# Performance work log

Hardware: AMD Instinct MI355X
Metric: run time of the kernel (lower is better)

Reference implementation:

```python
import jax, jax.numpy as jnp
import numpy as np
from jax import lax

B, C, H, W = 8, 128, 128, 128
HEADS = 16
HEAD_C = C // HEADS  # 8
SLOPE = 0.2
EPS = 1e-12


def _conv(x, w, b, padding, groups=1):
    # x: [B,C,H,W], w: [O,I/groups,kh,kw]
    y = lax.conv_general_dilated(
        x, w, window_strides=(1, 1), padding=padding,
        dimension_numbers=("NCHW", "OIHW", "NCHW"),
        feature_group_count=groups)
    return y + b[None, :, None, None]


def _conv_block(x, conv1_w, conv1_b, conv2_w, conv2_b, dw_w, dw_b, sc_w, sc_b):
    h = _conv(x, conv1_w, conv1_b, ((1, 1), (1, 1)))            # 3x3, zero pad
    h = jnp.where(h >= 0, h, SLOPE * h)                          # LeakyReLU
    h = _conv(h, conv2_w, conv2_b, ((0, 0), (0, 0)))             # 1x1
    hp = jnp.pad(h, ((0, 0), (0, 0), (1, 1), (1, 1)), mode="reflect")
    h = _conv(hp, dw_w, dw_b, ((0, 0), (0, 0)), groups=C)        # depthwise 3x3, reflect pad
    h = jnp.where(h >= 0, h, SLOPE * h)
    sc = _conv(x, sc_w, sc_b, ((0, 0), (0, 0)))                  # 1x1 shortcut
    return h + sc


def setup_inputs() -> dict:
    key = jax.random.key(0)
    ks = jax.random.split(key, 10)
    s = 0.05
    return {
        "x1": jax.random.normal(ks[0], (B, C, H, W), jnp.float32),
        "x2": jax.random.normal(ks[1], (B, C, H, W), jnp.float32),
        "temperature": jnp.ones((HEADS, 1, 1), jnp.float32),
        "conv1_w": jax.random.normal(ks[2], (C, C, 3, 3), jnp.float32) * s,
        "conv1_b": jnp.zeros((C,), jnp.float32),
        "conv2_w": jax.random.normal(ks[3], (C, C, 1, 1), jnp.float32) * s,
        "conv2_b": jnp.zeros((C,), jnp.float32),
        "dw_w": jax.random.normal(ks[4], (C, 1, 3, 3), jnp.float32) * s,
        "dw_b": jnp.zeros((C,), jnp.float32),
        "sc_w": jax.random.normal(ks[5], (C, C, 1, 1), jnp.float32) * s,
        "sc_b": jnp.zeros((C,), jnp.float32),
    }


def reference(x1, x2, temperature, conv1_w, conv1_b, conv2_w, conv2_b,
              dw_w, dw_b, sc_w, sc_b):
    b, c, h, w = x2.shape
    # b (head c) h w -> b head c (h w)
    qk = x1.reshape(b, HEADS, HEAD_C, h * w)
    v = x2.reshape(b, HEADS, HEAD_C, h * w)
    # L2-normalize over spatial dim (F.normalize, eps=1e-12)
    norm = jnp.sqrt(jnp.sum(qk * qk, axis=-1, keepdims=True))
    qn = qk / jnp.maximum(norm, EPS)
    # channel attention: [b, head, c, c]
    attn = jnp.einsum("bhcn,bhdn->bhcd", qn, qn) * temperature
    attn = jax.nn.softmax(attn, axis=-1)
    out = jnp.einsum("bhcd,bhdn->bhcn", attn, v)
    out = out.reshape(b, c, h, w)
    out = _conv_block(out, conv1_w, conv1_b, conv2_w, conv2_b,
                      dw_w, dw_b, sc_w, sc_b)
    return out + x1
```

## Files before the change

### kernel.cpp

```cpp
#include <hip/hip_runtime.h>
#include <hip/hip_bf16.h>

typedef __attribute__((ext_vector_type(8))) short short8;
typedef __attribute__((ext_vector_type(4))) float f32x4;

#define NB 8
#define NC 128
#define NHW 128
#define NSP (NHW*NHW)
#define SLOPE 0.2f
#define EPSN 1e-12f

static __device__ __forceinline__ unsigned short f2bf(float f) {
    __hip_bfloat16 h = __float2bfloat16(f);
    return *reinterpret_cast<unsigned short*>(&h);
}
static __device__ __forceinline__ float bf2f(__hip_bfloat16 h) {
    return __bfloat162float(h);
}

__global__ void prep_wb1(const float* __restrict__ w, __hip_bfloat16* __restrict__ wb) {
    int idx = blockIdx.x * 256 + threadIdx.x;
    if (idx >= 128 * 128 * 9) return;
    int kw = idx % 3; int t = idx / 3;
    int kh = t % 3;   t /= 3;
    int i  = t % 128; int o = t / 128;
    int tap = kh * 3 + kw;
    int q = i >> 5, lk = (i >> 3) & 3, j = i & 7;
    int wn = o >> 6, c = (o >> 4) & 3, l15 = o & 15;
    int lane = lk * 16 + l15;
    size_t chunk = ((size_t)(tap * 4 + q) * 2 + wn) * 4 + c;
    wb[chunk * 512 + lane * 8 + j] = __float2bfloat16(w[idx]);
}

__global__ void prep_w1x1(const float* __restrict__ w, __hip_bfloat16* __restrict__ wb) {
    int idx = blockIdx.x * 256 + threadIdx.x;
    if (idx >= 128 * 128) return;
    int i = idx & 127, o = idx >> 7;
    int kk = i >> 5, lk = (i >> 3) & 3, j = i & 7;
    int wn = o >> 6, c = (o >> 4) & 3, l15 = o & 15;
    int lane = lk * 16 + l15;
    size_t chunk = ((size_t)(wn * 4 + kk) * 4 + c);
    wb[chunk * 512 + lane * 8 + j] = __float2bfloat16(w[idx]);
}

__global__ __launch_bounds__(256) void gram_part(const float* __restrict__ x1,
                                                 float* __restrict__ Gp) {
    int bh = blockIdx.x & 127;
    int q  = blockIdx.x >> 7;
    const float* base = x1 + (size_t)bh * 8 * NSP + q * 4096;
    float acc[8][8];
#pragma unroll
    for (int c = 0; c < 8; c++)
#pragma unroll
        for (int d = 0; d < 8; d++) acc[c][d] = 0.f;

    for (int n = threadIdx.x; n < 4096; n += 256) {
        float v[8];
#pragma unroll
        for (int c = 0; c < 8; c++) v[c] = base[c * NSP + n];
#pragma unroll
        for (int c = 0; c < 8; c++)
#pragma unroll
            for (int d = 0; d < 8; d++)
                acc[c][d] = fmaf(v[c], v[d], acc[c][d]);
    }
#pragma unroll
    for (int c = 0; c < 8; c++)
#pragma unroll
        for (int d = 0; d < 8; d++)
            for (int off = 32; off > 0; off >>= 1)
                acc[c][d] += __shfl_down(acc[c][d], off);

    __shared__ float red[4][64];
    int wv = threadIdx.x >> 6;
    if ((threadIdx.x & 63) == 0) {
#pragma unroll
        for (int c = 0; c < 8; c++)
#pragma unroll
            for (int d = 0; d < 8; d++) red[wv][c * 8 + d] = acc[c][d];
    }
    __syncthreads();
    if (threadIdx.x < 64)
        Gp[(size_t)(q * 128 + bh) * 64 + threadIdx.x] =
            red[0][threadIdx.x] + red[1][threadIdx.x] + red[2][threadIdx.x] + red[3][threadIdx.x];
}

__global__ void gram_reduce(const float* __restrict__ Gp, float* __restrict__ G) {
    int bh = blockIdx.x;
    int t = threadIdx.x;
    float s = 0.f;
#pragma unroll
    for (int q = 0; q < 4; q++) s += Gp[(size_t)(q * 128 + bh) * 64 + t];
    G[bh * 64 + t] = s;
}

__global__ void softmax_kernel(const float* __restrict__ G, const float* __restrict__ temp,
                               float* __restrict__ attn) {
    int bh = blockIdx.x; int h = bh & 15;
    int t = threadIdx.x;
    int c = t >> 3, d = t & 7;
    const float* g = G + bh * 64;
    float nc = fmaxf(sqrtf(g[c * 8 + c]), EPSN);
    float nd = fmaxf(sqrtf(g[d * 8 + d]), EPSN);
    float a = g[t] / (nc * nd) * temp[h];
    float m = a;
#pragma unroll
    for (int off = 4; off > 0; off >>= 1) m = fmaxf(m, __shfl_xor(m, off));
    float e = __expf(a - m);
    float s = e;
#pragma unroll
    for (int off = 4; off > 0; off >>= 1) s += __shfl_xor(s, off);
    attn[bh * 64 + t] = e / s;
}

__global__ __launch_bounds__(256) void av_v2(const float* __restrict__ x2,
                                             const float* __restrict__ attn,
                                             __hip_bfloat16* __restrict__ yt) {
    int b  = blockIdx.x >> 8;
    int p0 = (blockIdx.x & 255) << 6;
    __shared__ float vt[128][65];
    __shared__ float at[16][65];
    for (int idx = threadIdx.x; idx < 1024; idx += 256)
        at[idx >> 6][idx & 63] = attn[(size_t)b * 1024 + idx];
    for (int idx = threadIdx.x; idx < 8192; idx += 256) {
        int row = idx >> 6, col = idx & 63;
        vt[row][col] = x2[(size_t)(b * 128 + row) * NSP + p0 + col];
    }
    __syncthreads();
    for (int idx = threadIdx.x; idx < 1024; idx += 256) {
        int cq = idx & 15;
        int p  = idx >> 4;
        float vv[8];
#pragma unroll
        for (int d = 0; d < 8; d++) vv[d] = vt[cq * 8 + d][p];
        unsigned int pk[4];
#pragma unroll
        for (int c = 0; c < 8; c += 2) {
            float s0 = 0.f, s1 = 0.f;
#pragma unroll
            for (int d = 0; d < 8; d++) {
                s0 = fmaf(at[cq][c * 8 + d], vv[d], s0);
                s1 = fmaf(at[cq][(c + 1) * 8 + d], vv[d], s1);
            }
            pk[c >> 1] = (unsigned int)f2bf(s0) | ((unsigned int)f2bf(s1) << 16);
        }
        uint4 st; st.x = pk[0]; st.y = pk[1]; st.z = pk[2]; st.w = pk[3];
        *reinterpret_cast<uint4*>(yt + ((size_t)b * NSP + p0 + p) * 128 + cq * 8) = st;
    }
}

__global__ __launch_bounds__(256, 4) void fused_conv(const __hip_bfloat16* __restrict__ yt,
                                                     const __hip_bfloat16* __restrict__ wb1,
                                                     const __hip_bfloat16* __restrict__ wb2,
                                                     const __hip_bfloat16* __restrict__ wbsc,
                                                     const float* __restrict__ b1,
                                                     const float* __restrict__ b2,
                                                     const float* __restrict__ bsc,
                                                     const float* __restrict__ x1,
                                                     __hip_bfloat16* __restrict__ h2,
                                                     float* __restrict__ out) {
    __shared__ uint4 smem[2048];
    char* smem_raw = (char*)smem;
    int bid = blockIdx.x;
    int blk = (bid & 7) * 128 + (bid >> 3);
    int b = blk >> 7, h = blk & 127;
    int tid = threadIdx.x;
    int lane = tid & 63;
    int wid = tid >> 6;
    int wm = wid >> 1, wn = wid & 1;
    int l15 = lane & 15;
    int lk = lane >> 4;

    const short8* wf1  = reinterpret_cast<const short8*>(wb1);
    const short8* wf2  = reinterpret_cast<const short8*>(wb2);
    const short8* wfsc = reinterpret_cast<const short8*>(wbsc);

    f32x4 acc[4][4];
#pragma unroll
    for (int a = 0; a < 4; a++)
#pragma unroll
        for (int c = 0; c < 4; c++) acc[a][c] = (f32x4){0.f, 0.f, 0.f, 0.f};

#pragma unroll
    for (int q = 0; q < 4; ++q) {
        __syncthreads();
        for (int idx = tid; idx < 1584; idx += 256) {
            int g = idx & 3;
            int colr = idx >> 2;
            int col = colr % 132;
            int r = colr / 132;
            int hh = h + r - 1;
            int w = col - 1;
            uint4 v = make_uint4(0u, 0u, 0u, 0u);
            if ((unsigned)hh < 128u && (unsigned)w < 128u)
                v = *reinterpret_cast<const uint4*>(
                    yt + (((size_t)(b * 128 + hh)) * 128 + w) * 128 + q * 32 + g * 8);
            smem[r * 528 + col * 4 + (g ^ (col & 3))] = v;
        }
        __syncthreads();

#pragma unroll
        for (int tap = 0; tap < 9; ++tap) {
            int kh = tap / 3, kw = tap - kh * 3;
            const short8* wp = wf1 + ((size_t)((tap * 4 + q) * 2 + wn) * 4) * 64 + lane;
            short8 bfr[4];
#pragma unroll
            for (int c = 0; c < 4; ++c)
                bfr[c] = wp[c * 64];
            short8 afr[4];
#pragma unroll
            for (int a = 0; a < 4; ++a) {
                int col = (wm * 4 + a) * 16 + l15 + kw;
                afr[a] = *reinterpret_cast<const short8*>(
                    &smem[kh * 528 + col * 4 + (lk ^ (col & 3))]);
            }
#pragma unroll
            for (int a = 0; a < 4; ++a)
#pragma unroll
                for (int c = 0; c < 4; ++c)
                    acc[a][c] = __builtin_amdgcn_mfma_f32_16x16x32_bf16(
                        afr[a], bfr[c], acc[a][c], 0, 0, 0);
        }
    }

    __syncthreads();
#pragma unroll
    for (int c = 0; c < 4; ++c) {
        int o = wn * 64 + c * 16 + l15;
        float bv = b1[o];
        int go = o >> 3, ob = (o & 7) << 1;
#pragma unroll
        for (int a = 0; a < 4; ++a) {
            int pb = (wm * 4 + a) * 16 + lk * 4;
#pragma unroll
            for (int j = 0; j < 4; ++j) {
                int p = pb + j;
                float v = acc[a][c][j] + bv;
                v = v >= 0.f ? v : SLOPE * v;
                *reinterpret_cast<__hip_bfloat16*>(
                    smem_raw + p * 256 + (((go ^ (p & 15)) << 4) | ob)) = __float2bfloat16(v);
            }
        }
    }
    __syncthreads();

#pragma unroll
    for (int a = 0; a < 4; a++)
#pragma unroll
        for (int c = 0; c < 4; c++) acc[a][c] = (f32x4){0.f, 0.f, 0.f, 0.f};
#pragma unroll
    for (int kk = 0; kk < 4; ++kk) {
        short8 bfr[4];
#pragma unroll
        for (int c = 0; c < 4; ++c)
            bfr[c] = wf2[((size_t)(wn * 4 + kk) * 4 + c) * 64 + lane];
        short8 afr[4];
        int g = kk * 4 + lk;
#pragma unroll
        for (int a = 0; a < 4; ++a) {
            int p = (wm * 4 + a) * 16 + l15;
            afr[a] = *reinterpret_cast<const short8*>(smem_raw + p * 256 + ((g ^ (p & 15)) << 4));
        }
#pragma unroll
        for (int a = 0; a < 4; ++a)
#pragma unroll
            for (int c = 0; c < 4; ++c)
                acc[a][c] = __builtin_amdgcn_mfma_f32_16x16x32_bf16(afr[a], bfr[c], acc[a][c], 0, 0, 0);
    }
#pragma unroll
    for (int c = 0; c < 4; ++c) {
        int o = wn * 64 + c * 16 + l15;
        float bv = b2[o];
        size_t obase = ((size_t)(b * 128 + o) * 128 + h) * 128;
#pragma unroll
        for (int a = 0; a < 4; ++a) {
            int w0 = (wm * 4 + a) * 16 + lk * 4;
            uint2 st;
            st.x = (unsigned int)f2bf(acc[a][c][0] + bv) | ((unsigned int)f2bf(acc[a][c][1] + bv) << 16);
            st.y = (unsigned int)f2bf(acc[a][c][2] + bv) | ((unsigned int)f2bf(acc[a][c][3] + bv) << 16);
            *reinterpret_cast<uint2*>(h2 + obase + w0) = st;
        }
    }

    __syncthreads();
    for (int idx = tid; idx < 2048; idx += 256) {
        int p = idx >> 4, g = idx & 15;
        uint4 v = *reinterpret_cast<const uint4*>(
            yt + ((size_t)(b * NSP + h * 128 + p)) * 128 + g * 8);
        *reinterpret_cast<uint4*>(smem_raw + p * 256 + ((g ^ (p & 15)) << 4)) = v;
    }
    __syncthreads();

#pragma unroll
    for (int a = 0; a < 4; a++)
#pragma unroll
        for (int c = 0; c < 4; c++) acc[a][c] = (f32x4){0.f, 0.f, 0.f, 0.f};
#pragma unroll
    for (int kk = 0; kk < 4; ++kk) {
        short8 bfr[4];
#pragma unroll
        for (int c = 0; c < 4; ++c)
            bfr[c] = wfsc[((size_t)(wn * 4 + kk) * 4 + c) * 64 + lane];
        short8 afr[4];
        int g = kk * 4 + lk;
#pragma unroll
        for (int a = 0; a < 4; ++a) {
            int p = (wm * 4 + a) * 16 + l15;
            afr[a] = *reinterpret_cast<const short8*>(smem_raw + p * 256 + ((g ^ (p & 15)) << 4));
        }
#pragma unroll
        for (int a = 0; a < 4; ++a)
#pragma unroll
            for (int c = 0; c < 4; ++c)
                acc[a][c] = __builtin_amdgcn_mfma_f32_16x16x32_bf16(afr[a], bfr[c], acc[a][c], 0, 0, 0);
    }
#pragma unroll
    for (int c = 0; c < 4; ++c) {
        int o = wn * 64 + c * 16 + l15;
        float bv = bsc[o];
        size_t obase = ((size_t)(b * 128 + o) * 128 + h) * 128;
#pragma unroll
        for (int a = 0; a < 4; ++a) {
            int w0 = (wm * 4 + a) * 16 + lk * 4;
            float4 xv = *reinterpret_cast<const float4*>(x1 + obase + w0);
            float4 st;
            st.x = acc[a][c][0] + bv + xv.x;
            st.y = acc[a][c][1] + bv + xv.y;
            st.z = acc[a][c][2] + bv + xv.z;
            st.w = acc[a][c][3] + bv + xv.w;
            *reinterpret_cast<float4*>(out + obase + w0) = st;
        }
    }
}

__global__ __launch_bounds__(256) void dw_v2(const __hip_bfloat16* __restrict__ h2,
                                             const float* __restrict__ dww,
                                             const float* __restrict__ dwb,
                                             float* __restrict__ out) {
    int bid = blockIdx.x;
    int swz = (bid & 7) * 1024 + (bid >> 3);
    size_t tidx = (size_t)swz * 256 + threadIdx.x;
    int w0 = (int)((tidx & 15) << 3);
    int hh = (int)((tidx >> 4) & 127);
    int bc = (int)(tidx >> 11);
    int c  = bc & 127;
    const __hip_bfloat16* src = h2 + ((size_t)bc << 14);
    float wg[9];
#pragma unroll
    for (int k = 0; k < 9; ++k) wg[k] = dww[c * 9 + k];
    float bv = dwb[c];
    float a8[8];
#pragma unroll
    for (int j = 0; j < 8; ++j) a8[j] = bv;
#pragma unroll
    for (int kh = 0; kh < 3; ++kh) {
        int ih = hh + kh - 1;
        ih = ih < 0 ? 1 : (ih > 127 ? 126 : ih);
        const __hip_bfloat16* row = src + ih * 128;
        short8 mid = *reinterpret_cast<const short8*>(row + w0);
        float v[10];
        v[0] = bf2f(row[w0 == 0 ? 1 : w0 - 1]);
#pragma unroll
        for (int j = 0; j < 8; ++j)
            v[j + 1] = __uint_as_float((unsigned int)(unsigned short)mid[j] << 16);
        v[9] = bf2f(row[w0 == 120 ? 126 : w0 + 8]);
#pragma unroll
        for (int kw = 0; kw < 3; ++kw)
#pragma unroll
            for (int j = 0; j < 8; ++j)
                a8[j] = fmaf(v[j + kw], wg[kh * 3 + kw], a8[j]);
    }
    size_t ob = ((size_t)bc << 14) + hh * 128 + w0;
    float4 o0 = *reinterpret_cast<const float4*>(out + ob);
    float4 o1 = *reinterpret_cast<const float4*>(out + ob + 4);
#pragma unroll
    for (int j = 0; j < 8; ++j) a8[j] = a8[j] >= 0.f ? a8[j] : SLOPE * a8[j];
    o0.x += a8[0]; o0.y += a8[1]; o0.z += a8[2]; o0.w += a8[3];
    o1.x += a8[4]; o1.y += a8[5]; o1.z += a8[6]; o1.w += a8[7];
    *reinterpret_cast<float4*>(out + ob) = o0;
    *reinterpret_cast<float4*>(out + ob + 4) = o1;
}

extern "C" void kernel_launch(void* const* d_in, const int* in_sizes, int n_in,
                              void* d_out, int out_size, void* d_ws, size_t ws_size,
                              hipStream_t stream) {
    const float* x1   = (const float*)d_in[0];
    const float* x2   = (const float*)d_in[1];
    const float* temp = (const float*)d_in[2];
    const float* c1w  = (const float*)d_in[3];
    const float* c1b  = (const float*)d_in[4];
    const float* c2w  = (const float*)d_in[5];
    const float* c2b  = (const float*)d_in[6];
    const float* dww  = (const float*)d_in[7];
    const float* dwb  = (const float*)d_in[8];
    const float* scw  = (const float*)d_in[9];
    const float* scb  = (const float*)d_in[10];
    float* out = (float*)d_out;
    char* ws = (char*)d_ws;

    float*          G    = (float*)(ws);
    float*          attn = (float*)(ws + (32 << 10));
    float*          Gp   = (float*)(ws + (64 << 10));
    __hip_bfloat16* wb1  = (__hip_bfloat16*)(ws + (192 << 10));
    __hip_bfloat16* wb2  = (__hip_bfloat16*)(ws + (480 << 10));
    __hip_bfloat16* wbsc = (__hip_bfloat16*)(ws + (512 << 10));
    __hip_bfloat16* yt   = (__hip_bfloat16*)(ws + ((size_t)1 << 20));
    __hip_bfloat16* h2b  = (__hip_bfloat16*)(ws + ((size_t)34 << 20));

    prep_wb1<<<576, 256, 0, stream>>>(c1w, wb1);
    prep_w1x1<<<64, 256, 0, stream>>>(c2w, wb2);
    prep_w1x1<<<64, 256, 0, stream>>>(scw, wbsc);

    gram_part<<<512, 256, 0, stream>>>(x1, Gp);
    gram_reduce<<<128, 64, 0, stream>>>(Gp, G);
    softmax_kernel<<<128, 64, 0, stream>>>(G, temp, attn);
    av_v2<<<2048, 256, 0, stream>>>(x2, attn, yt);

    fused_conv<<<1024, 256, 0, stream>>>(yt, wb1, wb2, wbsc, c1b, c2b, scb, x1, h2b, out);
    dw_v2<<<8192, 256, 0, stream>>>(h2b, dww, dwb, out);
}
```

Measured before the change: 167.9 us.

## Prefetch conv weights across taps, unswizzle LDS layout, raise MFMA priority

The 3x3 conv loop now loads the next tap's weight fragments into registers while the current tap's MFMAs run, so global load latency can overlap with compute. The LDS staging layout changes from an XOR-swizzled per-column layout to a plane-per-k-group layout, [(r*4+g)*132+col], to simplify addressing and change the bank access pattern. MFMA blocks are wrapped in s_setprio to favour matrix issue, and launch bounds drop from 4 to 3 waves per SIMD, which gives more registers for the prefetch buffers at the cost of occupancy.

```diff
diff --git a/kernel.cpp b/kernel.cpp
--- a/kernel.cpp
+++ b/kernel.cpp
@@ -150,7 +150,7 @@
     }
 }
 
-__global__ __launch_bounds__(256, 4) void fused_conv(const __hip_bfloat16* __restrict__ yt,
+__global__ __launch_bounds__(256, 3) void fused_conv(const __hip_bfloat16* __restrict__ yt,
                                                      const __hip_bfloat16* __restrict__ wb1,
                                                      const __hip_bfloat16* __restrict__ wb2,
                                                      const __hip_bfloat16* __restrict__ wbsc,
@@ -196,31 +196,37 @@
             if ((unsigned)hh < 128u && (unsigned)w < 128u)
                 v = *reinterpret_cast<const uint4*>(
                     yt + (((size_t)(b * 128 + hh)) * 128 + w) * 128 + q * 32 + g * 8);
-            smem[r * 528 + col * 4 + (g ^ (col & 3))] = v;
+            smem[(r * 4 + g) * 132 + col] = v;
         }
         __syncthreads();
+
+        const short8* wp0 = wf1 + ((size_t)((0 * 4 + q) * 2 + wn) * 4) * 64 + lane;
+        short8 cb0 = wp0[0], cb1 = wp0[64], cb2 = wp0[128], cb3 = wp0[192];
 
 #pragma unroll
         for (int tap = 0; tap < 9; ++tap) {
             int kh = tap / 3, kw = tap - kh * 3;
-            const short8* wp = wf1 + ((size_t)((tap * 4 + q) * 2 + wn) * 4) * 64 + lane;
-            short8 bfr[4];
-#pragma unroll
-            for (int c = 0; c < 4; ++c)
-                bfr[c] = wp[c * 64];
+            short8 nb0, nb1, nb2, nb3;
+            if (tap < 8) {
+                const short8* wpn = wf1 + ((size_t)(((tap + 1) * 4 + q) * 2 + wn) * 4) * 64 + lane;
+                nb0 = wpn[0]; nb1 = wpn[64]; nb2 = wpn[128]; nb3 = wpn[192];
+            }
             short8 afr[4];
 #pragma unroll
             for (int a = 0; a < 4; ++a) {
                 int col = (wm * 4 + a) * 16 + l15 + kw;
-                afr[a] = *reinterpret_cast<const short8*>(
-                    &smem[kh * 528 + col * 4 + (lk ^ (col & 3))]);
+                afr[a] = *reinterpret_cast<const short8*>(&smem[(kh * 4 + lk) * 132 + col]);
             }
-#pragma unroll
-            for (int a = 0; a < 4; ++a)
-#pragma unroll
-                for (int c = 0; c < 4; ++c)
-                    acc[a][c] = __builtin_amdgcn_mfma_f32_16x16x32_bf16(
-                        afr[a], bfr[c], acc[a][c], 0, 0, 0);
+            __builtin_amdgcn_s_setprio(1);
+#pragma unroll
+            for (int a = 0; a < 4; ++a) {
+                acc[a][0] = __builtin_amdgcn_mfma_f32_16x16x32_bf16(afr[a], cb0, acc[a][0], 0, 0, 0);
+                acc[a][1] = __builtin_amdgcn_mfma_f32_16x16x32_bf16(afr[a], cb1, acc[a][1], 0, 0, 0);
+                acc[a][2] = __builtin_amdgcn_mfma_f32_16x16x32_bf16(afr[a], cb2, acc[a][2], 0, 0, 0);
+                acc[a][3] = __builtin_amdgcn_mfma_f32_16x16x32_bf16(afr[a], cb3, acc[a][3], 0, 0, 0);
+            }
+            __builtin_amdgcn_s_setprio(0);
+            if (tap < 8) { cb0 = nb0; cb1 = nb1; cb2 = nb2; cb3 = nb3; }
         }
     }
 
@@ -262,11 +268,13 @@
             int p = (wm * 4 + a) * 16 + l15;
             afr[a] = *reinterpret_cast<const short8*>(smem_raw + p * 256 + ((g ^ (p & 15)) << 4));
         }
+        __builtin_amdgcn_s_setprio(1);
 #pragma unroll
         for (int a = 0; a < 4; ++a)
 #pragma unroll
             for (int c = 0; c < 4; ++c)
                 acc[a][c] = __builtin_amdgcn_mfma_f32_16x16x32_bf16(afr[a], bfr[c], acc[a][c], 0, 0, 0);
+        __builtin_amdgcn_s_setprio(0);
     }
 #pragma unroll
     for (int c = 0; c < 4; ++c) {
@@ -309,11 +317,13 @@
             int p = (wm * 4 + a) * 16 + l15;
             afr[a] = *reinterpret_cast<const short8*>(smem_raw + p * 256 + ((g ^ (p & 15)) << 4));
         }
+        __builtin_amdgcn_s_setprio(1);
 #pragma unroll
         for (int a = 0; a < 4; ++a)
 #pragma unroll
             for (int c = 0; c < 4; ++c)
                 acc[a][c] = __builtin_amdgcn_mfma_f32_16x16x32_bf16(afr[a], bfr[c], acc[a][c], 0, 0, 0);
+        __builtin_amdgcn_s_setprio(0);
     }
 #pragma unroll
     for (int c = 0; c < 4; ++c) {
```

Result: faster. 159.8 us (-4.8%).
